# Kernel tuning notes

Measured on AMD Instinct MI355X. Metric: run time of the kernel, lower is better.

## Reference

```python
import jax, jax.numpy as jnp
import numpy as np
from jax import lax

B, OBS, E, H = 65536, 20, 64, 64


def setup_inputs() -> dict:
    key = jax.random.key(0)
    ks = jax.random.split(key, 13)
    s = 0.1
    inp = {
        "obs_traj": jax.random.normal(ks[0], (B, OBS, 2), jnp.float32),
        "W_emb": jax.random.normal(ks[1], (E, 2), jnp.float32) * s,
        "b_emb": jax.random.normal(ks[2], (E,), jnp.float32) * s,
        "Wih_e": jax.random.normal(ks[3], (4 * H, E), jnp.float32) * s,
        "Whh_e": jax.random.normal(ks[4], (4 * H, H), jnp.float32) * s,
        "bih_e": jax.random.normal(ks[5], (4 * H,), jnp.float32) * s,
        "bhh_e": jax.random.normal(ks[6], (4 * H,), jnp.float32) * s,
        "Wih_d": jax.random.normal(ks[7], (4 * H, E), jnp.float32) * s,
        "Whh_d": jax.random.normal(ks[8], (4 * H, H), jnp.float32) * s,
        "bih_d": jax.random.normal(ks[9], (4 * H,), jnp.float32) * s,
        "bhh_d": jax.random.normal(ks[10], (4 * H,), jnp.float32) * s,
        "W_fc": jax.random.normal(ks[11], (2, H), jnp.float32) * s,
        "b_fc": jax.random.normal(ks[12], (2,), jnp.float32) * s,
        "pred_len": 12,
    }
    return inp


def _lstm_step(x, h, c, Wih, Whh, b):
    # PyTorch LSTM gate order: i, f, g, o
    g = x @ Wih.T + h @ Whh.T + b  # [B, 4H]
    i, f, gg, o = jnp.split(g, 4, axis=-1)
    c2 = jax.nn.sigmoid(f) * c + jax.nn.sigmoid(i) * jnp.tanh(gg)
    h2 = jax.nn.sigmoid(o) * jnp.tanh(c2)
    return h2, c2


def reference(obs_traj, W_emb, b_emb, Wih_e, Whh_e, bih_e, bhh_e,
              Wih_d, Whh_d, bih_d, bhh_d, W_fc, b_fc, pred_len):
    bsz = obs_traj.shape[0]
    dt = obs_traj.dtype
    # Encoder: embed all observed steps at once, then scan the LSTM over time.
    emb = jax.nn.relu(obs_traj @ W_emb.T + b_emb)  # [B, OBS, E]
    b_e = bih_e + bhh_e
    h0 = jnp.zeros((bsz, H), dt)
    c0 = jnp.zeros((bsz, H), dt)

    def enc_step(carry, x_t):
        h, c = carry
        h, c = _lstm_step(x_t, h, c, Wih_e, Whh_e, b_e)
        return (h, c), None

    (h, c), _ = lax.scan(enc_step, (h0, c0), jnp.swapaxes(emb, 0, 1))

    b_d = bih_d + bhh_d
    dec_in = jax.nn.relu(obs_traj[:, -1, :] @ W_emb.T + b_emb)  # [B, E]

    def dec_step(carry, _):
        h, c, x = carry
        h, c = _lstm_step(x, h, c, Wih_d, Whh_d, b_d)
        pred = h @ W_fc.T + b_fc  # [B, 2]
        nxt = jax.nn.relu(pred @ W_emb.T + b_emb)
        return (h, c, nxt), pred

    _, preds = lax.scan(dec_step, (h, c, dec_in), None, length=pred_len)
    return jnp.swapaxes(preds, 0, 1)  # [B, pred_len, 2]
```

## Files before the change

kernel.cpp:

```cpp
#include <hip/hip_runtime.h>

typedef __bf16 bf16x8 __attribute__((ext_vector_type(8)));
typedef __bf16 bf16x4 __attribute__((ext_vector_type(4)));
typedef float  f32x4  __attribute__((ext_vector_type(4)));
typedef float  f32x2  __attribute__((ext_vector_type(2)));

constexpr int OBS   = 20;
constexpr int PRED  = 12;
constexpr int AST   = 136;
constexpr int NBIG  = 512;
constexpr int GRID  = 768;

constexpr float SIO = -1.4426950408889634f;
constexpr float SG  =  2.8853900817779268f;

__device__ __forceinline__ float exp2_(float x) { return __builtin_amdgcn_exp2f(x); }
__device__ __forceinline__ float rcp_(float x)  { return __builtin_amdgcn_rcpf(x); }

struct SmallW {
    float  biasf_e[256];
    float  biasf_d[256];
    float4 embc[64];
    float  wfc[128];
    float  bfc[2];
};

__device__ __forceinline__ void load_bfr(bf16x8 (&bfr)[4][3],
                                         const float* Wih, const float* Whh,
                                         int wblk, int m, int q) {
    #pragma unroll
    for (int c = 0; c < 4; ++c) {
        const float sc = (c == 2) ? SG : SIO;
        const int n = c * 64 + wblk + m;
        #pragma unroll
        for (int kt = 0; kt < 3; ++kt) {
            const float* s = (kt < 2) ? (Wih + n * 64 + kt * 32 + q * 8)
                                      : (Whh + n * 64 + q * 8);
            float4 a = *(const float4*)s;
            float4 b = *(const float4*)(s + 4);
            bf16x8 v;
            v[0] = (__bf16)(sc * a.x); v[1] = (__bf16)(sc * a.y);
            v[2] = (__bf16)(sc * a.z); v[3] = (__bf16)(sc * a.w);
            v[4] = (__bf16)(sc * b.x); v[5] = (__bf16)(sc * b.y);
            v[6] = (__bf16)(sc * b.z); v[7] = (__bf16)(sc * b.w);
            bfr[c][kt] = v;
        }
    }
}

__device__ __forceinline__ void fill_wkt3(bf16x8* wkt3, const float* Whh,
                                          int wv, int lane, int wblk, int m, int q) {
    #pragma unroll
    for (int c = 0; c < 4; ++c) {
        const float sc = (c == 2) ? SG : SIO;
        const int n = c * 64 + wblk + m;
        const float* s = Whh + n * 64 + 32 + q * 8;
        float4 a = *(const float4*)s;
        float4 b = *(const float4*)(s + 4);
        bf16x8 v;
        v[0] = (__bf16)(sc * a.x); v[1] = (__bf16)(sc * a.y);
        v[2] = (__bf16)(sc * a.z); v[3] = (__bf16)(sc * a.w);
        v[4] = (__bf16)(sc * b.x); v[5] = (__bf16)(sc * b.y);
        v[6] = (__bf16)(sc * b.z); v[7] = (__bf16)(sc * b.w);
        wkt3[(wv * 4 + c) * 64 + lane] = v;
    }
}

template<int NSUB>
__device__ void lstm_body(__bf16* As, bf16x8* wkt3, SmallW& sw,
                          const float* obs,
                          const float* Wih_e, const float* Whh_e,
                          const float* Wih_d, const float* Whh_d,
                          float* out, size_t gRow0)
{
    constexpr int CH = NSUB * 16;
    constexpr int NP = (NSUB + 1) / 2;
    const int tid  = threadIdx.x;
    const int wv   = tid >> 6;
    const int lane = tid & 63;
    const int m    = lane & 15;
    const int q    = lane >> 4;
    const int wblk = wv * 16;

    bf16x8 bfr[4][3];
    load_bfr(bfr, Wih_e, Whh_e, wblk, m, q);

    f32x4 cst[2 * NSUB];
    #pragma unroll
    for (int i = 0; i < 2 * NSUB; ++i) cst[i] = f32x4{0.f, 0.f, 0.f, 0.f};

    f32x4 acc[NSUB][4];

    auto gemm = [&](int chunk, const float* bfrag) {
        #pragma unroll
        for (int c = 0; c < 4; ++c) {
            f32x4 b = *(const f32x4*)&bfrag[(wv * 4 + c) * 16 + q * 4];
            #pragma unroll
            for (int s = 0; s < NSUB; ++s) acc[s][c] = b;
        }
        #pragma unroll
        for (int kt = 0; kt < 3; ++kt) {
            bf16x8 af[NSUB];
            #pragma unroll
            for (int s = 0; s < NSUB; ++s)
                af[s] = *(const bf16x8*)&As[(chunk * CH + s * 16 + m) * AST + kt * 32 + q * 8];
            #pragma unroll
            for (int s = 0; s < NSUB; ++s)
                #pragma unroll
                for (int c = 0; c < 4; ++c)
                    acc[s][c] = __builtin_amdgcn_mfma_f32_16x16x32_bf16(bfr[c][kt], af[s], acc[s][c], 0, 0, 0);
        }
        {
            bf16x8 af[NSUB];
            #pragma unroll
            for (int s = 0; s < NSUB; ++s)
                af[s] = *(const bf16x8*)&As[(chunk * CH + s * 16 + m) * AST + 96 + q * 8];
            #pragma unroll
            for (int c = 0; c < 4; ++c) {
                bf16x8 w3 = wkt3[(wv * 4 + c) * 64 + lane];
                #pragma unroll
                for (int s = 0; s < NSUB; ++s)
                    acc[s][c] = __builtin_amdgcn_mfma_f32_16x16x32_bf16(w3, af[s], acc[s][c], 0, 0, 0);
            }
        }
    };

    auto update = [&](int chunk) {
        #pragma unroll
        for (int sub = 0; sub < NSUB; ++sub) {
            const int idx = chunk * NSUB + sub;
            const int row = chunk * CH + sub * 16 + m;
            f32x4 ci = cst[idx];
            bf16x4 h4;
            #pragma unroll
            for (int r = 0; r < 4; ++r) {
                const float gi = acc[sub][0][r];
                const float gf = acc[sub][1][r];
                const float gg = acc[sub][2][r];
                const float go = acc[sub][3][r];
                const float Ef = exp2_(gf);
                const float a  = ci[r] * rcp_(1.0f + Ef);
                const float Ei = exp2_(gi);
                const float Eg = exp2_(gg);
                const float d1 = 1.0f + Ei;
                const float r1 = rcp_(fmaf(d1, Eg, d1));
                const float cN = fmaf(Eg - 1.0f, r1, a);
                const float Eo = exp2_(go);
                const float Ec = exp2_(cN * SG);
                const float d2 = 1.0f + Eo;
                const float r2 = rcp_(fmaf(d2, Ec, d2));
                const float h  = (Ec - 1.0f) * r2;
                ci[r] = cN;
                h4[r] = (__bf16)h;
            }
            cst[idx] = ci;
            *(bf16x4*)&As[row * AST + 64 + wblk + q * 4] = h4;
        }
    };

    auto load_obs = [&](int chunk, int t, f32x2* ov) {
        #pragma unroll
        for (int p = 0; p < NP; ++p) {
            const int rloc = p * 32 + (lane & 31);
            if (rloc < CH)
                ov[p] = *(const f32x2*)(obs + (gRow0 + chunk * CH + rloc) * (OBS * 2) + t * 2);
        }
    };
    auto emb_store = [&](int chunk, const f32x2* ov) {
        const int h8 = lane >> 5;
        #pragma unroll
        for (int p = 0; p < NP; ++p) {
            const int rloc = p * 32 + (lane & 31);
            if (rloc < CH) {
                const int row = chunk * CH + rloc;
                bf16x8 v;
                #pragma unroll
                for (int j = 0; j < 8; ++j) {
                    float4 wc = sw.embc[wblk + h8 * 8 + j];
                    v[j] = (__bf16)fmaxf(fmaf(ov[p][0], wc.x, fmaf(ov[p][1], wc.y, wc.z)), 0.f);
                }
                *(bf16x8*)&As[row * AST + wblk + h8 * 8] = v;
            }
        }
    };

    __syncthreads();

    {
        f32x2 o0[NP], o1[NP];
        load_obs(0, 0, o0); load_obs(1, 0, o1);
        emb_store(0, o0);   emb_store(1, o1);
    }
    __syncthreads();
    gemm(0, sw.biasf_e);

    for (int t = 0; t < OBS; ++t) {
        __syncthreads();
        f32x2 ovA[NP];
        if (t + 1 < OBS) load_obs(0, t + 1, ovA);
        update(0);
        gemm(1, sw.biasf_e);
        if (t + 1 < OBS) emb_store(0, ovA);
        __syncthreads();
        f32x2 ovB[NP];
        if (t + 1 < OBS) load_obs(1, t + 1, ovB);
        update(1);
        if (t + 1 < OBS) {
            gemm(0, sw.biasf_e);
            emb_store(1, ovB);
        }
    }

    load_bfr(bfr, Wih_d, Whh_d, wblk, m, q);
    fill_wkt3(wkt3, Whh_d, wv, lane, wblk, m, q);

    bf16x8 wcf[2];
    {
        float4 we = sw.embc[wblk + m];
        #pragma unroll
        for (int kt = 0; kt < 2; ++kt) {
            bf16x8 v;
            #pragma unroll
            for (int j = 0; j < 8; ++j) {
                const int k = kt * 32 + q * 8 + j;
                v[j] = (__bf16)(we.x * sw.wfc[k] + we.y * sw.wfc[64 + k]);
            }
            wcf[kt] = v;
        }
    }
    f32x4 bcf;
    #pragma unroll
    for (int r = 0; r < 4; ++r) {
        float4 wc = sw.embc[wblk + q * 4 + r];
        bcf[r] = wc.x * sw.bfc[0] + wc.y * sw.bfc[1] + wc.z;
    }

    auto emb_gemm = [&](int chunk) {
        #pragma unroll
        for (int s = 0; s < NSUB; ++s) {
            const int row = chunk * CH + s * 16 + m;
            f32x4 a = bcf;
            #pragma unroll
            for (int kt = 0; kt < 2; ++kt) {
                bf16x8 hf = *(const bf16x8*)&As[row * AST + 64 + kt * 32 + q * 8];
                a = __builtin_amdgcn_mfma_f32_16x16x32_bf16(wcf[kt], hf, a, 0, 0, 0);
            }
            bf16x4 x4;
            #pragma unroll
            for (int r = 0; r < 4; ++r) x4[r] = (__bf16)fmaxf(a[r], 0.f);
            *(bf16x4*)&As[row * AST + wblk + q * 4] = x4;
        }
    };

    auto pred_phase = [&](int chunk, int td) {
        const int comp = (tid >> 2) & 1;
        const int seg  = tid & 3;
        #pragma unroll
        for (int p = 0; p < NP; ++p) {
            const int rloc = p * 32 + (tid >> 3);
            const int row  = chunk * CH + rloc;
            const bool act = (rloc < CH);
            float pv = 0.f;
            if (act) {
                bf16x8 h0 = *(const bf16x8*)&As[row * AST + 64 + seg * 16];
                bf16x8 h1 = *(const bf16x8*)&As[row * AST + 64 + seg * 16 + 8];
                f32x4 w0 = *(const f32x4*)&sw.wfc[comp * 64 + seg * 16];
                f32x4 w1 = *(const f32x4*)&sw.wfc[comp * 64 + seg * 16 + 4];
                f32x4 w2 = *(const f32x4*)&sw.wfc[comp * 64 + seg * 16 + 8];
                f32x4 w3 = *(const f32x4*)&sw.wfc[comp * 64 + seg * 16 + 12];
                pv = (float)h0[0] * w0[0] + (float)h0[1] * w0[1] + (float)h0[2] * w0[2] + (float)h0[3] * w0[3]
                   + (float)h0[4] * w1[0] + (float)h0[5] * w1[1] + (float)h0[6] * w1[2] + (float)h0[7] * w1[3]
                   + (float)h1[0] * w2[0] + (float)h1[1] * w2[1] + (float)h1[2] * w2[2] + (float)h1[3] * w2[3]
                   + (float)h1[4] * w3[0] + (float)h1[5] * w3[1] + (float)h1[6] * w3[2] + (float)h1[7] * w3[3];
            }
            pv += __shfl_xor(pv, 1, 64);
            pv += __shfl_xor(pv, 2, 64);
            if (act && seg == 0) {
                pv += sw.bfc[comp];
                out[((gRow0 + row) * PRED + td) * 2 + comp] = pv;
            }
        }
    };

    gemm(0, sw.biasf_d);

    for (int td = 0; td < PRED; ++td) {
        __syncthreads();
        update(0);
        gemm(1, sw.biasf_d);
        __syncthreads();
        update(1);
        if (td + 1 < PRED) emb_gemm(0);
        pred_phase(0, td);
        __syncthreads();
        if (td + 1 < PRED) {
            emb_gemm(1);
            gemm(0, sw.biasf_d);
        }
        pred_phase(1, td);
    }
}

__global__ __launch_bounds__(256, 3)
void vanilla_lstm(const float* __restrict__ obs,
                  const float* __restrict__ W_emb, const float* __restrict__ b_emb,
                  const float* __restrict__ Wih_e, const float* __restrict__ Whh_e,
                  const float* __restrict__ bih_e, const float* __restrict__ bhh_e,
                  const float* __restrict__ Wih_d, const float* __restrict__ Whh_d,
                  const float* __restrict__ bih_d, const float* __restrict__ bhh_d,
                  const float* __restrict__ W_fc,  const float* __restrict__ b_fc,
                  float* __restrict__ out)
{
    __shared__ __align__(16) __bf16 As[96 * AST];
    __shared__ bf16x8 wkt3[1024];
    __shared__ SmallW sw;

    const int tid = threadIdx.x;

    {
        const int wv_ = tid >> 6, c_ = (tid >> 4) & 3, qr = tid & 15;
        const int g = c_ * 64 + wv_ * 16 + qr;
        const float sc = (c_ == 2) ? SG : SIO;
        sw.biasf_e[tid] = sc * (bih_e[g] + bhh_e[g]);
        sw.biasf_d[tid] = sc * (bih_d[g] + bhh_d[g]);
    }
    if (tid < 64)  sw.embc[tid] = make_float4(W_emb[2 * tid], W_emb[2 * tid + 1], b_emb[tid], 0.f);
    if (tid < 128) sw.wfc[tid]  = W_fc[tid];
    if (tid < 2)   sw.bfc[tid]  = b_fc[tid];

    {
        uint4 z; z.x = z.y = z.z = z.w = 0u;
        #pragma unroll
        for (int i = 0; i < 3; ++i) {
            const int idx = tid + i * 256;
            const int r = idx >> 3, o = idx & 7;
            *((uint4*)&As[r * AST + 64] + o) = z;
        }
    }

    {
        const int wv = tid >> 6, lane = tid & 63, m = lane & 15, q = lane >> 4;
        fill_wkt3(wkt3, Whh_e, wv, lane, wv * 16, m, q);
    }

    const int bid = blockIdx.x;
    if (bid < NBIG) {
        lstm_body<3>(As, wkt3, sw, obs, Wih_e, Whh_e, Wih_d, Whh_d,
                     out, (size_t)bid * 96);
    } else {
        lstm_body<2>(As, wkt3, sw, obs, Wih_e, Whh_e, Wih_d, Whh_d,
                     out, (size_t)NBIG * 96 + (size_t)(bid - NBIG) * 64);
    }
}

extern "C" void kernel_launch(void* const* d_in, const int* in_sizes, int n_in,
                              void* d_out, int out_size, void* d_ws, size_t ws_size,
                              hipStream_t stream) {
    (void)in_sizes; (void)n_in; (void)d_ws; (void)ws_size; (void)out_size;
    const float* obs   = (const float*)d_in[0];
    const float* W_emb = (const float*)d_in[1];
    const float* b_emb = (const float*)d_in[2];
    const float* Wih_e = (const float*)d_in[3];
    const float* Whh_e = (const float*)d_in[4];
    const float* bih_e = (const float*)d_in[5];
    const float* bhh_e = (const float*)d_in[6];
    const float* Wih_d = (const float*)d_in[7];
    const float* Whh_d = (const float*)d_in[8];
    const float* bih_d = (const float*)d_in[9];
    const float* bhh_d = (const float*)d_in[10];
    const float* W_fc  = (const float*)d_in[11];
    const float* b_fc  = (const float*)d_in[12];
    float* o = (float*)d_out;

    dim3 grid(GRID), block(256);
    hipLaunchKernelGGL(vanilla_lstm, grid, block, 0, stream,
                       obs, W_emb, b_emb, Wih_e, Whh_e, bih_e, bhh_e,
                       Wih_d, Whh_d, bih_d, bhh_d, W_fc, b_fc, o);
}
```

Measured before the change: 271.8 us.

## Fuse decoder prediction into embedding MFMA pass and stagger block start

Merges the output projection into the embedding pass. It reuses the same hidden-state LDS loads and computes the two prediction components with a padded MFMA instead of scalar dot products and shuffles. It also rewrites the cell update to use a single reciprocal for the combined forget and input-gate terms. Blocks now sleep for a role-dependent time at startup to stagger the phases of co-resident blocks. Costs are extra MFMA issue on one wave per subtile, a possible overflow risk from the product of three exp terms, and idle startup cycles.

```diff
diff --git a/kernel.cpp b/kernel.cpp
--- a/kernel.cpp
+++ b/kernel.cpp
@@ -139,12 +139,13 @@
                 const float gg = acc[sub][2][r];
                 const float go = acc[sub][3][r];
                 const float Ef = exp2_(gf);
-                const float a  = ci[r] * rcp_(1.0f + Ef);
                 const float Ei = exp2_(gi);
                 const float Eg = exp2_(gg);
-                const float d1 = 1.0f + Ei;
-                const float r1 = rcp_(fmaf(d1, Eg, d1));
-                const float cN = fmaf(Eg - 1.0f, r1, a);
+                const float pf = 1.0f + Ef;
+                const float t1 = (1.0f + Ei) * (1.0f + Eg);
+                const float R  = rcp_(pf * t1);
+                const float num = fmaf(ci[r], t1, (Eg - 1.0f) * pf);
+                const float cN = num * R;
                 const float Eo = exp2_(go);
                 const float Ec = exp2_(cN * SG);
                 const float d2 = 1.0f + Eo;
@@ -234,50 +235,42 @@
         float4 wc = sw.embc[wblk + q * 4 + r];
         bcf[r] = wc.x * sw.bfc[0] + wc.y * sw.bfc[1] + wc.z;
     }
-
-    auto emb_gemm = [&](int chunk) {
+    bf16x8 wfcf[2];
+    #pragma unroll
+    for (int kt = 0; kt < 2; ++kt) {
+        bf16x8 v;
+        #pragma unroll
+        for (int j = 0; j < 8; ++j) v[j] = (__bf16)0.f;
+        if (m < 2) {
+            #pragma unroll
+            for (int j = 0; j < 8; ++j)
+                v[j] = (__bf16)sw.wfc[m * 64 + kt * 32 + q * 8 + j];
+        }
+        wfcf[kt] = v;
+    }
+    const float bfc0 = sw.bfc[0], bfc1 = sw.bfc[1];
+
+    auto embpred = [&](int chunk, int td, bool doEmb) {
         #pragma unroll
         for (int s = 0; s < NSUB; ++s) {
             const int row = chunk * CH + s * 16 + m;
-            f32x4 a = bcf;
-            #pragma unroll
-            for (int kt = 0; kt < 2; ++kt) {
-                bf16x8 hf = *(const bf16x8*)&As[row * AST + 64 + kt * 32 + q * 8];
-                a = __builtin_amdgcn_mfma_f32_16x16x32_bf16(wcf[kt], hf, a, 0, 0, 0);
-            }
-            bf16x4 x4;
-            #pragma unroll
-            for (int r = 0; r < 4; ++r) x4[r] = (__bf16)fmaxf(a[r], 0.f);
-            *(bf16x4*)&As[row * AST + wblk + q * 4] = x4;
-        }
-    };
-
-    auto pred_phase = [&](int chunk, int td) {
-        const int comp = (tid >> 2) & 1;
-        const int seg  = tid & 3;
-        #pragma unroll
-        for (int p = 0; p < NP; ++p) {
-            const int rloc = p * 32 + (tid >> 3);
-            const int row  = chunk * CH + rloc;
-            const bool act = (rloc < CH);
-            float pv = 0.f;
-            if (act) {
-                bf16x8 h0 = *(const bf16x8*)&As[row * AST + 64 + seg * 16];
-                bf16x8 h1 = *(const bf16x8*)&As[row * AST + 64 + seg * 16 + 8];
-                f32x4 w0 = *(const f32x4*)&sw.wfc[comp * 64 + seg * 16];
-                f32x4 w1 = *(const f32x4*)&sw.wfc[comp * 64 + seg * 16 + 4];
-                f32x4 w2 = *(const f32x4*)&sw.wfc[comp * 64 + seg * 16 + 8];
-                f32x4 w3 = *(const f32x4*)&sw.wfc[comp * 64 + seg * 16 + 12];
-                pv = (float)h0[0] * w0[0] + (float)h0[1] * w0[1] + (float)h0[2] * w0[2] + (float)h0[3] * w0[3]
-                   + (float)h0[4] * w1[0] + (float)h0[5] * w1[1] + (float)h0[6] * w1[2] + (float)h0[7] * w1[3]
-                   + (float)h1[0] * w2[0] + (float)h1[1] * w2[1] + (float)h1[2] * w2[2] + (float)h1[3] * w2[3]
-                   + (float)h1[4] * w3[0] + (float)h1[5] * w3[1] + (float)h1[6] * w3[2] + (float)h1[7] * w3[3];
-            }
-            pv += __shfl_xor(pv, 1, 64);
-            pv += __shfl_xor(pv, 2, 64);
-            if (act && seg == 0) {
-                pv += sw.bfc[comp];
-                out[((gRow0 + row) * PRED + td) * 2 + comp] = pv;
+            bf16x8 hf0 = *(const bf16x8*)&As[row * AST + 64 + q * 8];
+            bf16x8 hf1 = *(const bf16x8*)&As[row * AST + 96 + q * 8];
+            if (doEmb) {
+                f32x4 a = bcf;
+                a = __builtin_amdgcn_mfma_f32_16x16x32_bf16(wcf[0], hf0, a, 0, 0, 0);
+                a = __builtin_amdgcn_mfma_f32_16x16x32_bf16(wcf[1], hf1, a, 0, 0, 0);
+                bf16x4 x4;
+                #pragma unroll
+                for (int r = 0; r < 4; ++r) x4[r] = (__bf16)fmaxf(a[r], 0.f);
+                *(bf16x4*)&As[row * AST + wblk + q * 4] = x4;
+            }
+            if (wv == s) {
+                f32x4 p = f32x4{bfc0, bfc1, 0.f, 0.f};
+                p = __builtin_amdgcn_mfma_f32_16x16x32_bf16(wfcf[0], hf0, p, 0, 0, 0);
+                p = __builtin_amdgcn_mfma_f32_16x16x32_bf16(wfcf[1], hf1, p, 0, 0, 0);
+                if (q == 0)
+                    *(f32x2*)&out[((gRow0 + row) * PRED + td) * 2] = f32x2{p[0], p[1]};
             }
         }
     };
@@ -285,19 +278,16 @@
     gemm(0, sw.biasf_d);
 
     for (int td = 0; td < PRED; ++td) {
+        const bool more = (td + 1 < PRED);
         __syncthreads();
         update(0);
         gemm(1, sw.biasf_d);
         __syncthreads();
         update(1);
-        if (td + 1 < PRED) emb_gemm(0);
-        pred_phase(0, td);
-        __syncthreads();
-        if (td + 1 < PRED) {
-            emb_gemm(1);
-            gemm(0, sw.biasf_d);
-        }
-        pred_phase(1, td);
+        embpred(0, td, more);
+        __syncthreads();
+        embpred(1, td, more);
+        if (more) gemm(0, sw.biasf_d);
     }
 }
 
@@ -316,6 +306,12 @@
     __shared__ SmallW sw;
 
     const int tid = threadIdx.x;
+    const int bid = blockIdx.x;
+
+    {
+        const int role = (bid >> 8) % 3;
+        for (int i = 0; i < role; ++i) __builtin_amdgcn_s_sleep(50);
+    }
 
     {
         const int wv_ = tid >> 6, c_ = (tid >> 4) & 3, qr = tid & 15;
@@ -343,7 +339,6 @@
         fill_wkt3(wkt3, Whh_e, wv, lane, wv * 16, m, q);
     }
 
-    const int bid = blockIdx.x;
     if (bid < NBIG) {
         lstm_body<3>(As, wkt3, sw, obs, Wih_e, Whh_e, Wih_d, Whh_d,
                      out, (size_t)bid * 96);
```

Result: slower. 292.8 us (+7.7%).
